# Kernel optimization log

Hardware: AMD Instinct MI355X
Metric: run time of the kernel (lower is better)

The kernel has to match this reference:

```python
import jax, jax.numpy as jnp
import numpy as np

B, S, H = 4, 2048, 2048
N_HEADS, KV_HEADS, RANK = 16, 8, 64
HEAD_DIM = H // N_HEADS          # 128
N_REP = N_HEADS // KV_HEADS      # 2
NEG = -1e9


def setup_inputs() -> dict:
    key = jax.random.key(0)
    ks = jax.random.split(key, 6)
    hidden_states = jax.random.normal(ks[0], (B, S, H), dtype=jnp.float32)
    # additive causal mask, broadcast over heads: [B,1,S,S]
    causal = jnp.tril(jnp.ones((S, S), dtype=bool))
    attention_mask = jnp.where(causal, 0.0, NEG).astype(jnp.float32)
    attention_mask = jnp.broadcast_to(attention_mask[None, None], (B, 1, S, S))
    sc = 1.0 / np.sqrt(H)
    Wq = jax.random.normal(ks[1], (H, RANK), dtype=jnp.float32) * sc
    Wk = jax.random.normal(ks[2], (H, RANK), dtype=jnp.float32) * sc
    Wv = jax.random.normal(ks[3], (H, KV_HEADS * HEAD_DIM), dtype=jnp.float32) * sc
    Wo = jax.random.normal(ks[4], (H, H), dtype=jnp.float32) * sc
    return {"hidden_states": hidden_states, "attention_mask": attention_mask,
            "Wq": Wq, "Wk": Wk, "Wv": Wv, "Wo": Wo}


def reference(hidden_states, attention_mask, Wq, Wk, Wv, Wo):
    b, s, h = hidden_states.shape
    # low-rank CP factors shared across heads: [B,S,R]
    q = hidden_states @ Wq
    k = hidden_states @ Wk
    # values with GQA: [B, kv_heads, S, head_dim] -> repeat to [B, n_heads, S, head_dim]
    v = (hidden_states @ Wv).reshape(b, s, KV_HEADS, HEAD_DIM).transpose(0, 2, 1, 3)
    v = jnp.repeat(v, N_REP, axis=1)
    # CP circuit over the (i,j) grid: scores[b,i,j] = sum_r q[b,i,r] * k[b,j,r]
    # (Hadamard over embedding factors gathered at grid indices, SumLayer with unit
    #  weights over rank; the all-ones head factor multiplies by 1). Head-shared.
    scores = jnp.einsum('bir,bjr->bij', q, k)[:, None]  # [B,1,S,S]
    scores = scores + attention_mask                     # additive causal mask
    probs = jax.nn.softmax(scores.astype(jnp.float32), axis=-1).astype(v.dtype)
    # attn_probs @ V, broadcasting the head-shared probs over heads
    ctx = jnp.einsum('bij,bhjd->bhid', probs[:, 0], v)   # [B,H,S,D]
    ctx = ctx.transpose(0, 2, 1, 3).reshape(b, s, h)
    return ctx @ Wo
```

## Files before the change

### kernel.cpp

```cpp
#include <hip/hip_runtime.h>

#define B_ 4
#define S_ 2048
#define H_ 2048
#define R_ 64
#define DKV_ 1024

typedef __attribute__((ext_vector_type(8))) short s16x8;
typedef __attribute__((ext_vector_type(4))) float f32x4v;

__device__ __forceinline__ unsigned short f2bf(float x) {
  unsigned int u = __builtin_bit_cast(unsigned int, x);
  u += 0x7FFF + ((u >> 16) & 1);
  return (unsigned short)(u >> 16);
}
__device__ __forceinline__ float bf2f(unsigned short h) {
  unsigned int u = ((unsigned int)h) << 16;
  return __builtin_bit_cast(float, u);
}

__device__ __forceinline__ void gl_lds16(const void* g, void* l) {
  __builtin_amdgcn_global_load_lds(
      (const __attribute__((address_space(1))) unsigned int*)g,
      (__attribute__((address_space(3))) unsigned int*)l, 16, 0, 0);
}

__device__ __forceinline__ int swz_off(int m, int kb) {
  int L = m >> 1;
  int slot = ((m & 1) << 2) | (kb >> 4);
  int sp = slot ^ (L & 7);
  return (L << 7) | (sp << 4) | (kb & 15);
}

__global__ __launch_bounds__(256) void k_f32_to_bf16x2(const float* __restrict__ in,
    unsigned short* __restrict__ hi, unsigned short* __restrict__ lo, int n4) {
  int i = blockIdx.x * 256 + threadIdx.x;
  if (i >= n4) return;
  float4 v = ((const float4*)in)[i];
  ushort4 h, l;
  h.x = f2bf(v.x); h.y = f2bf(v.y); h.z = f2bf(v.z); h.w = f2bf(v.w);
  l.x = f2bf(v.x - bf2f(h.x)); l.y = f2bf(v.y - bf2f(h.y));
  l.z = f2bf(v.z - bf2f(h.z)); l.w = f2bf(v.w - bf2f(h.w));
  ((ushort4*)hi)[i] = h;
  ((ushort4*)lo)[i] = l;
}

__global__ __launch_bounds__(256) void k_transpose_bf16(const float* __restrict__ in,
    unsigned short* __restrict__ out, int rows, int cols) {
  __shared__ float tile[32][33];
  int c0 = blockIdx.x * 32, r0 = blockIdx.y * 32;
  int tx = threadIdx.x & 31, ty = threadIdx.x >> 5;
  for (int i = 0; i < 4; ++i)
    tile[ty + i * 8][tx] = in[(size_t)(r0 + ty + i * 8) * cols + c0 + tx];
  __syncthreads();
  for (int i = 0; i < 4; ++i)
    out[(size_t)(c0 + ty + i * 8) * rows + r0 + tx] = f2bf(tile[tx][ty + i * 8]);
}

__global__ __launch_bounds__(256) void k_build_wqkt(const float* __restrict__ Wq,
    const float* __restrict__ Wk, unsigned short* __restrict__ hiT,
    unsigned short* __restrict__ loT) {
  __shared__ float tile[32][33];
  int k0 = blockIdx.x * 32, n0 = blockIdx.y * 32;
  const float* W = (n0 < 64) ? Wq : Wk;
  int nb = n0 & 63;
  int tx = threadIdx.x & 31, ty = threadIdx.x >> 5;
  for (int i = 0; i < 4; ++i)
    tile[ty + i * 8][tx] = W[(size_t)(k0 + ty + i * 8) * R_ + nb + tx];
  __syncthreads();
  for (int i = 0; i < 4; ++i) {
    float v = tile[tx][ty + i * 8];
    unsigned short h = f2bf(v);
    size_t idx = (size_t)(n0 + ty + i * 8) * H_ + k0 + tx;
    hiT[idx] = h;
    loT[idx] = f2bf(v - bf2f(h));
  }
}

__global__ __launch_bounds__(256) void k_build_wot(const float* __restrict__ Wo,
                                                   unsigned short* __restrict__ WoT) {
  __shared__ float tile[32][33];
  int n0 = blockIdx.x * 32, r0 = blockIdx.y * 32;
  int h1b = 256 * (r0 >> 7) + (r0 & 127);
  int tx = threadIdx.x & 31, ty = threadIdx.x >> 5;
  for (int i = 0; i < 4; ++i) {
    int dr = ty + i * 8;
    tile[dr][tx] = Wo[(size_t)(h1b + dr) * H_ + n0 + tx] +
                   Wo[(size_t)(h1b + 128 + dr) * H_ + n0 + tx];
  }
  __syncthreads();
  for (int i = 0; i < 4; ++i)
    WoT[(size_t)(n0 + ty + i * 8) * DKV_ + r0 + tx] = f2bf(tile[tx][ty + i * 8]);
}

__global__ __launch_bounds__(256) void k_qk_mfma(
    const unsigned short* __restrict__ Ahi, const unsigned short* __restrict__ Alo,
    const unsigned short* __restrict__ Bhi, const unsigned short* __restrict__ Blo,
    unsigned short* __restrict__ qkh, unsigned short* __restrict__ qkl) {
  constexpr int TQK = 20480;
  __shared__ __attribute__((aligned(16))) char lds[3 * TQK];
  int m0 = blockIdx.x * 32;
  int t = threadIdx.x;
  int lane = t & 63, wave = t >> 6;
  int lr = lane & 15, kb = (lane >> 4) << 4;

  auto stage = [&](int kt, int buf) {
    int k0 = kt << 5;
    char* base = &lds[buf * TQK];
    {
      int q = t & 127;
      int L = q >> 3;
      int slot = (q & 7) ^ (L & 7);
      int m = (L << 1) | (slot >> 2);
      int ke = (slot & 3) << 3;
      const unsigned short* src =
          (t < 128 ? Ahi : Alo) + (size_t)(m0 + m) * H_ + k0 + ke;
      gl_lds16(src, base + (t < 128 ? 0 : 2048) + q * 16);
    }
#pragma unroll
    for (int c = 0; c < 2; ++c) {
      int q = c * 256 + t;
      int L = q >> 3;
      int slot = (q & 7) ^ (L & 7);
      int n = (L << 1) | (slot >> 2);
      int ke = (slot & 3) << 3;
      gl_lds16(Bhi + (size_t)n * H_ + k0 + ke, base + 4096 + q * 16);
    }
#pragma unroll
    for (int c = 0; c < 2; ++c) {
      int q = c * 256 + t;
      int L = q >> 3;
      int slot = (q & 7) ^ (L & 7);
      int n = (L << 1) | (slot >> 2);
      int ke = (slot & 3) << 3;
      gl_lds16(Blo + (size_t)n * H_ + k0 + ke, base + 12288 + q * 16);
    }
  };

  f32x4v acc[2][2] = {};
  stage(0, 0);
  stage(1, 1);
  int cur = 0, nxt = 2;
  for (int kt = 0; kt < 64; ++kt) {
    __builtin_amdgcn_sched_barrier(0);
    if (kt < 63) asm volatile("s_waitcnt vmcnt(5)" ::: "memory");
    else asm volatile("s_waitcnt vmcnt(0)" ::: "memory");
    __builtin_amdgcn_s_barrier();
    __builtin_amdgcn_sched_barrier(0);
    if (kt + 2 < 64) stage(kt + 2, nxt);
    const char* base = &lds[cur * TQK];
    s16x8 ah[2], al[2], bh[2], bl[2];
#pragma unroll
    for (int m = 0; m < 2; ++m) {
      int o = swz_off(m * 16 + lr, kb);
      ah[m] = *(const s16x8*)(base + o);
      al[m] = *(const s16x8*)(base + 2048 + o);
    }
#pragma unroll
    for (int n = 0; n < 2; ++n) {
      int o = swz_off(wave * 32 + n * 16 + lr, kb);
      bh[n] = *(const s16x8*)(base + 4096 + o);
      bl[n] = *(const s16x8*)(base + 12288 + o);
    }
    __builtin_amdgcn_s_setprio(1);
#pragma unroll
    for (int m = 0; m < 2; ++m)
#pragma unroll
      for (int n = 0; n < 2; ++n) {
        acc[m][n] = __builtin_amdgcn_mfma_f32_16x16x32_bf16(ah[m], bh[n], acc[m][n], 0, 0, 0);
        acc[m][n] = __builtin_amdgcn_mfma_f32_16x16x32_bf16(ah[m], bl[n], acc[m][n], 0, 0, 0);
        acc[m][n] = __builtin_amdgcn_mfma_f32_16x16x32_bf16(al[m], bh[n], acc[m][n], 0, 0, 0);
      }
    __builtin_amdgcn_s_setprio(0);
    cur = (cur == 2) ? 0 : cur + 1;
    nxt = (nxt == 2) ? 0 : nxt + 1;
  }
  for (int m = 0; m < 2; ++m) {
    int lrow = m * 16 + ((lane >> 4) << 2);
    for (int n = 0; n < 2; ++n) {
      int lcol = wave * 32 + n * 16 + lr;
      for (int r = 0; r < 4; ++r) {
        float v = acc[m][n][r];
        unsigned short h = f2bf(v);
        size_t idx = (size_t)(m0 + lrow + r) * 128 + lcol;
        qkh[idx] = h;
        qkl[idx] = f2bf(v - bf2f(h));
      }
    }
  }
}

__global__ __launch_bounds__(512, 4) void k_attn_fused(
    const unsigned short* __restrict__ qkh, const unsigned short* __restrict__ qkl,
    const unsigned short* __restrict__ VT, unsigned short* __restrict__ ctx) {
  constexpr int TILEB = 24576;
  __shared__ __attribute__((aligned(16))) char lds[3 * TILEB + 4096 + 256];
  char* Pt = &lds[3 * TILEB];
  float* rs = (float*)&lds[3 * TILEB + 4096];

  int t = threadIdx.x;
  int gx = gridDim.x;
  int x = blockIdx.x;
  int bx = (x & 1) ? (gx - 1 - (x >> 1)) : (x >> 1);
  if (blockIdx.z & 2) bx = gx - 1 - bx;
  int z = blockIdx.z;
  int m0 = bx * 64, d0 = blockIdx.y * 256;

  int lane = t & 63, wave = t >> 6;
  int sm = wave >> 1, sn = wave & 1;
  int wr = wave >> 2, wc = wave & 3;
  int kb = (lane >> 4) << 4;

  const unsigned short* qh = qkh + (size_t)z * S_ * 128;
  const unsigned short* ql = qkl + (size_t)z * S_ * 128;

  s16x8 qfh[2], qfl[2];
  {
    size_t rq = (size_t)(m0 + sm * 16 + (lane & 15)) * 128 + ((lane >> 4) << 3);
    qfh[0] = *(const s16x8*)(qh + rq);
    qfh[1] = *(const s16x8*)(qh + rq + 32);
    qfl[0] = *(const s16x8*)(ql + rq);
    qfl[1] = *(const s16x8*)(ql + rq + 32);
  }

  auto stage = [&](int kt, int buf) {
    int j0 = kt << 5;
    char* base = &lds[buf * TILEB];
    {
      int q = t & 127;
      int L = q >> 3;
      int slot = (q & 7) ^ (L & 7);
      int jr = (L << 1) | (slot >> 2);
      int ke = (slot & 3) << 3;
      int sub = t >> 7;
      const unsigned short* src = ((sub < 2) ? qh : ql) +
          (size_t)(j0 + jr) * 128 + 64 + ((sub & 1) << 5) + ke;
      gl_lds16(src, base + sub * 2048 + q * 16);
    }
    char* vb = base + 8192;
#pragma unroll
    for (int c = 0; c < 2; ++c) {
      int q = c * 512 + t;
      int L = q >> 3;
      int slot = (q & 7) ^ (L & 7);
      int dr = (L << 1) | (slot >> 2);
      int ke = (slot & 3) << 3;
      gl_lds16(VT + (size_t)(d0 + dr) * (B_ * S_) + (size_t)z * S_ + j0 + ke,
               vb + q * 16);
    }
  };

  if (t < 64) rs[t] = 0.f;
  int NT = (m0 + 64) >> 5;
  stage(0, 0);
  stage(1, 1);

  int jrow = sn * 16 + (lane & 15);
  int koffs = swz_off(jrow, kb);
  int paoff[2], voff[4];
#pragma unroll
  for (int mf = 0; mf < 2; ++mf)
    paoff[mf] = swz_off(wr * 32 + mf * 16 + (lane & 15), kb);
#pragma unroll
  for (int nf = 0; nf < 4; ++nf)
    voff[nf] = swz_off(wc * 64 + nf * 16 + (lane & 15), kb);

  float ps[4] = {0.f, 0.f, 0.f, 0.f};
  f32x4v accp[2][4] = {};
  int prow = sm * 16 + ((lane >> 4) << 2);
  int pcol = sn * 16 + (lane & 15);

  int cur = 0, nxt = 2;
  for (int kt = 0; kt < NT; ++kt) {
    __builtin_amdgcn_sched_barrier(0);
    if (kt + 1 < NT) asm volatile("s_waitcnt vmcnt(3) lgkmcnt(0)" ::: "memory");
    else asm volatile("s_waitcnt vmcnt(0) lgkmcnt(0)" ::: "memory");
    __builtin_amdgcn_s_barrier();
    __builtin_amdgcn_sched_barrier(0);
    if (kt + 2 < NT) stage(kt + 2, nxt);
    const char* base = &lds[cur * TILEB];
    s16x8 kh[2], kl[2];
    kh[0] = *(const s16x8*)(base + koffs);
    kh[1] = *(const s16x8*)(base + 2048 + koffs);
    kl[0] = *(const s16x8*)(base + 4096 + koffs);
    kl[1] = *(const s16x8*)(base + 6144 + koffs);
    f32x4v s = {};
#pragma unroll
    for (int ks = 0; ks < 2; ++ks) {
      s = __builtin_amdgcn_mfma_f32_16x16x32_bf16(qfh[ks], kh[ks], s, 0, 0, 0);
      s = __builtin_amdgcn_mfma_f32_16x16x32_bf16(qfh[ks], kl[ks], s, 0, 0, 0);
      s = __builtin_amdgcn_mfma_f32_16x16x32_bf16(qfl[ks], kh[ks], s, 0, 0, 0);
    }
    int jg = (kt << 5) + pcol;
    int ig = m0 + prow;
#pragma unroll
    for (int r = 0; r < 4; ++r) {
      float p = (jg <= ig + r) ? __expf(s[r]) : 0.f;
      ps[r] += p;
      *(unsigned short*)(Pt + swz_off(prow + r, pcol * 2)) = f2bf(p);
    }
    __builtin_amdgcn_sched_barrier(0);
    asm volatile("s_waitcnt lgkmcnt(0)" ::: "memory");
    __builtin_amdgcn_s_barrier();
    __builtin_amdgcn_sched_barrier(0);
    s16x8 pa[2], vf[4];
#pragma unroll
    for (int mf = 0; mf < 2; ++mf) pa[mf] = *(const s16x8*)(Pt + paoff[mf]);
    const char* vbase = base + 8192;
#pragma unroll
    for (int nf = 0; nf < 4; ++nf) vf[nf] = *(const s16x8*)(vbase + voff[nf]);
    __builtin_amdgcn_s_setprio(1);
#pragma unroll
    for (int mf = 0; mf < 2; ++mf)
#pragma unroll
      for (int nf = 0; nf < 4; ++nf)
        accp[mf][nf] =
            __builtin_amdgcn_mfma_f32_16x16x32_bf16(pa[mf], vf[nf], accp[mf][nf], 0, 0, 0);
    __builtin_amdgcn_s_setprio(0);
    cur = (cur == 2) ? 0 : cur + 1;
    nxt = (nxt == 2) ? 0 : nxt + 1;
  }

#pragma unroll
  for (int r = 0; r < 4; ++r) {
    float v = ps[r];
    for (int msk = 1; msk < 16; msk <<= 1) v += __shfl_xor(v, msk, 64);
    if ((lane & 15) == 0) atomicAdd(&rs[prow + r], v);
  }
  __syncthreads();

  unsigned short* Cp = ctx + (size_t)(z * S_ + m0) * DKV_ + d0;
#pragma unroll
  for (int mf = 0; mf < 2; ++mf) {
    int lr0 = wr * 32 + mf * 16 + ((lane >> 4) << 2);
#pragma unroll
    for (int nf = 0; nf < 4; ++nf) {
      int lc = wc * 64 + nf * 16 + (lane & 15);
#pragma unroll
      for (int r = 0; r < 4; ++r) {
        float sc = 1.f / rs[lr0 + r];
        Cp[(size_t)(lr0 + r) * DKV_ + lc] = f2bf(accp[mf][nf][r] * sc);
      }
    }
  }
}

template <int BM, int BN, bool TRANS_OUT, bool OUT_BF16>
__global__ __launch_bounds__(512, 4) void k_gemm256(
    const unsigned short* __restrict__ A, int lda,
    const unsigned short* __restrict__ BT, int ldbt,
    void* __restrict__ C, int ldc, int K) {
  constexpr int ABYTES = BM * 64;
  constexpr int BBYTES = BN * 64;
  constexpr int TILEB = ABYTES + BBYTES;
  constexpr int WARPS_M = 4;
  constexpr int WARPS_N = 2;
  constexpr int WM = BM / WARPS_M;
  constexpr int WN = BN / WARPS_N;
  constexpr int MF = WM / 16;
  constexpr int NF = WN / 16;
  constexpr int LPS = BM / 128 + BN / 128;
  __shared__ __attribute__((aligned(16))) char lds[3 * TILEB];

  int t = threadIdx.x;
  int gx = gridDim.x;
  int id = blockIdx.y * gx + blockIdx.x;
  int cpx = gx >> 3;
  int xcd = id & 7, rr = id >> 3;
  int bx = xcd * cpx + rr % cpx;
  int by = rr / cpx;
  int m0 = bx * BM, n0 = by * BN;

  const unsigned short* Ab = A + (size_t)m0 * lda;
  const unsigned short* Bb = BT + (size_t)n0 * ldbt;

  int lane = t & 63, wave = t >> 6;
  int wr = wave / WARPS_N, wc = wave % WARPS_N;
  int kb = (lane >> 4) << 4;
  int aoff[MF], boff[NF];
#pragma unroll
  for (int mf = 0; mf < MF; ++mf)
    aoff[mf] = swz_off(wr * WM + mf * 16 + (lane & 15), kb);
#pragma unroll
  for (int nf = 0; nf < NF; ++nf)
    boff[nf] = swz_off(wc * WN + nf * 16 + (lane & 15), kb);

  int NT = K >> 5;

  auto stage = [&](int kt, int buf) {
    int k0 = kt << 5;
    char* la = &lds[buf * TILEB];
    char* lb = la + ABYTES;
#pragma unroll
    for (int c = 0; c < BM / 128; ++c) {
      int q = c * 512 + t;
      int L = q >> 3;
      int slot = (q & 7) ^ (L & 7);
      int m = (L << 1) | (slot >> 2);
      int ke = (slot & 3) << 3;
      gl_lds16(Ab + (size_t)m * lda + k0 + ke, la + q * 16);
    }
#pragma unroll
    for (int c = 0; c < BN / 128; ++c) {
      int q = c * 512 + t;
      int L = q >> 3;
      int slot = (q & 7) ^ (L & 7);
      int n = (L << 1) | (slot >> 2);
      int ke = (slot & 3) << 3;
      gl_lds16(Bb + (size_t)n * ldbt + k0 + ke, lb + q * 16);
    }
  };

  f32x4v acc[MF][NF] = {};
  stage(0, 0);
  if (NT > 1) stage(1, 1);
  int cur = 0, nxt = 2;
  for (int kt = 0; kt < NT; ++kt) {
    __builtin_amdgcn_sched_barrier(0);
    if (kt + 1 < NT) {
      if constexpr (LPS == 2) asm volatile("s_waitcnt vmcnt(2)" ::: "memory");
      else asm volatile("s_waitcnt vmcnt(3)" ::: "memory");
    } else {
      asm volatile("s_waitcnt vmcnt(0)" ::: "memory");
    }
    __builtin_amdgcn_s_barrier();
    __builtin_amdgcn_sched_barrier(0);
    if (kt + 2 < NT) stage(kt + 2, nxt);
    const char* la = &lds[cur * TILEB];
    const char* lb = la + ABYTES;
    s16x8 af[MF], bf[NF];
#pragma unroll
    for (int mf = 0; mf < MF; ++mf) af[mf] = *(const s16x8*)(la + aoff[mf]);
#pragma unroll
    for (int nf = 0; nf < NF; ++nf) bf[nf] = *(const s16x8*)(lb + boff[nf]);
    __builtin_amdgcn_s_setprio(1);
#pragma unroll
    for (int mf = 0; mf < MF; ++mf)
#pragma unroll
      for (int nf = 0; nf < NF; ++nf)
        acc[mf][nf] =
            __builtin_amdgcn_mfma_f32_16x16x32_bf16(af[mf], bf[nf], acc[mf][nf], 0, 0, 0);
    __builtin_amdgcn_s_setprio(0);
    cur = (cur == 2) ? 0 : cur + 1;
    nxt = (nxt == 2) ? 0 : nxt + 1;
  }

#pragma unroll
  for (int mf = 0; mf < MF; ++mf) {
    int lrow = wr * WM + mf * 16 + ((lane >> 4) << 2);
#pragma unroll
    for (int nf = 0; nf < NF; ++nf) {
      int lcol = wc * WN + nf * 16 + (lane & 15);
      f32x4v v = acc[mf][nf];
      if (TRANS_OUT) {
        ushort4 o;
        o.x = f2bf(v[0]); o.y = f2bf(v[1]); o.z = f2bf(v[2]); o.w = f2bf(v[3]);
        unsigned short* Cp = (unsigned short*)C;
        *(ushort4*)&Cp[(size_t)(n0 + lcol) * ldc + m0 + lrow] = o;
      } else {
#pragma unroll
        for (int r = 0; r < 4; ++r) {
          if (OUT_BF16) {
            unsigned short* Cp = (unsigned short*)C;
            Cp[(size_t)(m0 + lrow + r) * ldc + n0 + lcol] = f2bf(v[r]);
          } else {
            float* Cp = (float*)C;
            Cp[(size_t)(m0 + lrow + r) * ldc + n0 + lcol] = v[r];
          }
        }
      }
    }
  }
}

extern "C" void kernel_launch(void* const* d_in, const int* in_sizes, int n_in,
                              void* d_out, int out_size, void* d_ws, size_t ws_size,
                              hipStream_t stream) {
  const float* hs = (const float*)d_in[0];
  const float* Wq = (const float*)d_in[2];
  const float* Wk = (const float*)d_in[3];
  const float* Wv = (const float*)d_in[4];
  const float* Wo = (const float*)d_in[5];
  float* out = (float*)d_out;

  char* w = (char*)d_ws;
  unsigned short* hsb = (unsigned short*)w; w += (size_t)B_ * S_ * H_ * 2;
  unsigned short* hsl = (unsigned short*)w; w += (size_t)B_ * S_ * H_ * 2;
  unsigned short* WvT = (unsigned short*)w; w += (size_t)DKV_ * H_ * 2;
  unsigned short* WoT = (unsigned short*)w; w += (size_t)H_ * DKV_ * 2;
  unsigned short* WqkTh = (unsigned short*)w; w += (size_t)128 * H_ * 2;
  unsigned short* WqkTl = (unsigned short*)w; w += (size_t)128 * H_ * 2;
  unsigned short* VT  = (unsigned short*)w; w += (size_t)DKV_ * B_ * S_ * 2;
  unsigned short* ctx = (unsigned short*)w; w += (size_t)B_ * S_ * DKV_ * 2;
  unsigned short* qkh = (unsigned short*)w; w += (size_t)B_ * S_ * 128 * 2;
  unsigned short* qkl = (unsigned short*)w; w += (size_t)B_ * S_ * 128 * 2;

  k_f32_to_bf16x2<<<(B_ * S_ * H_ / 4 + 255) / 256, 256, 0, stream>>>(
      hs, hsb, hsl, B_ * S_ * H_ / 4);
  k_transpose_bf16<<<dim3(DKV_ / 32, H_ / 32), 256, 0, stream>>>(Wv, WvT, H_, DKV_);
  k_build_wot<<<dim3(H_ / 32, DKV_ / 32), 256, 0, stream>>>(Wo, WoT);
  k_build_wqkt<<<dim3(H_ / 32, 4), 256, 0, stream>>>(Wq, Wk, WqkTh, WqkTl);
  k_qk_mfma<<<B_ * S_ / 32, 256, 0, stream>>>(hsb, hsl, WqkTh, WqkTl, qkh, qkl);
  k_gemm256<256, 128, true, true>
      <<<dim3(B_ * S_ / 256, DKV_ / 128), 512, 0, stream>>>(
      hsb, H_, WvT, H_, VT, B_ * S_, H_);
  k_attn_fused<<<dim3(32, 4, B_), 512, 0, stream>>>(qkh, qkl, VT, ctx);
  k_gemm256<256, 128, false, false>
      <<<dim3(B_ * S_ / 256, H_ / 128), 512, 0, stream>>>(
      ctx, DKV_, WoT, DKV_, out, H_, DKV_);
}
```

Before: 201.8 us.

## Keep attention probabilities in registers via transposed QK MFMA feeding PV directly

The fused attention kernel now computes S^T (K as the A operand, Q as B), so each lane's score outputs already match the A-operand layout of a 16x16x16 bf16 MFMA. P can then feed the PV product straight from registers, with no LDS round-trip and no second block barrier per tile. Work is repartitioned so each wave owns 16 query rows and 128 output columns. Row sums are reduced with shuffles instead of LDS atomics, and the V tile now uses an unswizzled layout. The cost is redundant QK MFMAs (each wave recomputes the scores for its row block across the two column halves) and possible LDS bank conflicts on the narrower, unswizzled V reads.

Measured after the change: 225.6 us. +11.8%, slower.

```diff
diff --git a/kernel.cpp b/kernel.cpp
--- a/kernel.cpp
+++ b/kernel.cpp
@@ -7,6 +7,7 @@
 #define DKV_ 1024
 
 typedef __attribute__((ext_vector_type(8))) short s16x8;
+typedef __attribute__((ext_vector_type(4))) short s16x4;
 typedef __attribute__((ext_vector_type(4))) float f32x4v;
 
 __device__ __forceinline__ unsigned short f2bf(float x) {
@@ -194,9 +195,7 @@
     const unsigned short* __restrict__ qkh, const unsigned short* __restrict__ qkl,
     const unsigned short* __restrict__ VT, unsigned short* __restrict__ ctx) {
   constexpr int TILEB = 24576;
-  __shared__ __attribute__((aligned(16))) char lds[3 * TILEB + 4096 + 256];
-  char* Pt = &lds[3 * TILEB];
-  float* rs = (float*)&lds[3 * TILEB + 4096];
+  __shared__ __attribute__((aligned(16))) char lds[3 * TILEB];
 
   int t = threadIdx.x;
   int gx = gridDim.x;
@@ -207,8 +206,7 @@
   int m0 = bx * 64, d0 = blockIdx.y * 256;
 
   int lane = t & 63, wave = t >> 6;
-  int sm = wave >> 1, sn = wave & 1;
-  int wr = wave >> 2, wc = wave & 3;
+  int iq = wave & 3, wd = wave >> 2;
   int kb = (lane >> 4) << 4;
 
   const unsigned short* qh = qkh + (size_t)z * S_ * 128;
@@ -216,7 +214,7 @@
 
   s16x8 qfh[2], qfl[2];
   {
-    size_t rq = (size_t)(m0 + sm * 16 + (lane & 15)) * 128 + ((lane >> 4) << 3);
+    size_t rq = (size_t)(m0 + iq * 16 + (lane & 15)) * 128 + ((lane >> 4) << 3);
     qfh[0] = *(const s16x8*)(qh + rq);
     qfh[1] = *(const s16x8*)(qh + rq + 32);
     qfl[0] = *(const s16x8*)(ql + rq);
@@ -241,107 +239,89 @@
 #pragma unroll
     for (int c = 0; c < 2; ++c) {
       int q = c * 512 + t;
-      int L = q >> 3;
-      int slot = (q & 7) ^ (L & 7);
-      int dr = (L << 1) | (slot >> 2);
-      int ke = (slot & 3) << 3;
-      gl_lds16(VT + (size_t)(d0 + dr) * (B_ * S_) + (size_t)z * S_ + j0 + ke,
+      int dr = q >> 2, jc = (q & 3) << 3;
+      gl_lds16(VT + (size_t)(d0 + dr) * (B_ * S_) + (size_t)z * S_ + j0 + jc,
                vb + q * 16);
     }
   };
 
-  if (t < 64) rs[t] = 0.f;
   int NT = (m0 + 64) >> 5;
   stage(0, 0);
   stage(1, 1);
 
-  int jrow = sn * 16 + (lane & 15);
-  int koffs = swz_off(jrow, kb);
-  int paoff[2], voff[4];
-#pragma unroll
-  for (int mf = 0; mf < 2; ++mf)
-    paoff[mf] = swz_off(wr * 32 + mf * 16 + (lane & 15), kb);
-#pragma unroll
-  for (int nf = 0; nf < 4; ++nf)
-    voff[nf] = swz_off(wc * 64 + nf * 16 + (lane & 15), kb);
-
-  float ps[4] = {0.f, 0.f, 0.f, 0.f};
-  f32x4v accp[2][4] = {};
-  int prow = sm * 16 + ((lane >> 4) << 2);
-  int pcol = sn * 16 + (lane & 15);
+  int ko0 = swz_off(lane & 15, kb);
+  int ko1 = swz_off(16 + (lane & 15), kb);
+  float ps = 0.f;
+  f32x4v accp[8] = {};
+  int ig = m0 + iq * 16 + (lane & 15);
 
   int cur = 0, nxt = 2;
   for (int kt = 0; kt < NT; ++kt) {
     __builtin_amdgcn_sched_barrier(0);
-    if (kt + 1 < NT) asm volatile("s_waitcnt vmcnt(3) lgkmcnt(0)" ::: "memory");
-    else asm volatile("s_waitcnt vmcnt(0) lgkmcnt(0)" ::: "memory");
+    if (kt + 1 < NT) asm volatile("s_waitcnt vmcnt(3)" ::: "memory");
+    else asm volatile("s_waitcnt vmcnt(0)" ::: "memory");
     __builtin_amdgcn_s_barrier();
     __builtin_amdgcn_sched_barrier(0);
     if (kt + 2 < NT) stage(kt + 2, nxt);
     const char* base = &lds[cur * TILEB];
-    s16x8 kh[2], kl[2];
-    kh[0] = *(const s16x8*)(base + koffs);
-    kh[1] = *(const s16x8*)(base + 2048 + koffs);
-    kl[0] = *(const s16x8*)(base + 4096 + koffs);
-    kl[1] = *(const s16x8*)(base + 6144 + koffs);
-    f32x4v s = {};
-#pragma unroll
-    for (int ks = 0; ks < 2; ++ks) {
-      s = __builtin_amdgcn_mfma_f32_16x16x32_bf16(qfh[ks], kh[ks], s, 0, 0, 0);
-      s = __builtin_amdgcn_mfma_f32_16x16x32_bf16(qfh[ks], kl[ks], s, 0, 0, 0);
-      s = __builtin_amdgcn_mfma_f32_16x16x32_bf16(qfl[ks], kh[ks], s, 0, 0, 0);
-    }
-    int jg = (kt << 5) + pcol;
-    int ig = m0 + prow;
-#pragma unroll
-    for (int r = 0; r < 4; ++r) {
-      float p = (jg <= ig + r) ? __expf(s[r]) : 0.f;
-      ps[r] += p;
-      *(unsigned short*)(Pt + swz_off(prow + r, pcol * 2)) = f2bf(p);
-    }
-    __builtin_amdgcn_sched_barrier(0);
-    asm volatile("s_waitcnt lgkmcnt(0)" ::: "memory");
-    __builtin_amdgcn_s_barrier();
-    __builtin_amdgcn_sched_barrier(0);
-    s16x8 pa[2], vf[4];
-#pragma unroll
-    for (int mf = 0; mf < 2; ++mf) pa[mf] = *(const s16x8*)(Pt + paoff[mf]);
-    const char* vbase = base + 8192;
-#pragma unroll
-    for (int nf = 0; nf < 4; ++nf) vf[nf] = *(const s16x8*)(vbase + voff[nf]);
+    s16x4 pa[2];
+#pragma unroll
+    for (int h = 0; h < 2; ++h) {
+      int ko = h ? ko1 : ko0;
+      s16x8 kh0 = *(const s16x8*)(base + ko);
+      s16x8 kh1 = *(const s16x8*)(base + 2048 + ko);
+      s16x8 kl0 = *(const s16x8*)(base + 4096 + ko);
+      s16x8 kl1 = *(const s16x8*)(base + 6144 + ko);
+      f32x4v s = {};
+      s = __builtin_amdgcn_mfma_f32_16x16x32_bf16(kh0, qfh[0], s, 0, 0, 0);
+      s = __builtin_amdgcn_mfma_f32_16x16x32_bf16(kh1, qfh[1], s, 0, 0, 0);
+      s = __builtin_amdgcn_mfma_f32_16x16x32_bf16(kl0, qfh[0], s, 0, 0, 0);
+      s = __builtin_amdgcn_mfma_f32_16x16x32_bf16(kl1, qfh[1], s, 0, 0, 0);
+      s = __builtin_amdgcn_mfma_f32_16x16x32_bf16(kh0, qfl[0], s, 0, 0, 0);
+      s = __builtin_amdgcn_mfma_f32_16x16x32_bf16(kh1, qfl[1], s, 0, 0, 0);
+      int jb = (kt << 5) + h * 16 + ((lane >> 4) << 2);
+      s16x4 p;
+#pragma unroll
+      for (int r = 0; r < 4; ++r) {
+        float pv = (jb + r <= ig) ? __expf(s[r]) : 0.f;
+        ps += pv;
+        p[r] = (short)f2bf(pv);
+      }
+      pa[h] = p;
+    }
+    const char* vb = base + 8192;
+    int jby = (lane >> 4) << 3;
     __builtin_amdgcn_s_setprio(1);
 #pragma unroll
-    for (int mf = 0; mf < 2; ++mf)
-#pragma unroll
-      for (int nf = 0; nf < 4; ++nf)
-        accp[mf][nf] =
-            __builtin_amdgcn_mfma_f32_16x16x32_bf16(pa[mf], vf[nf], accp[mf][nf], 0, 0, 0);
+    for (int nf = 0; nf < 8; ++nf) {
+      int dl = wd * 128 + nf * 16 + (lane & 15);
+#pragma unroll
+      for (int h = 0; h < 2; ++h) {
+        s16x4 vf = *(const s16x4*)(vb + dl * 64 + h * 32 + jby);
+        asm volatile("v_mfma_f32_16x16x16_bf16 %0, %1, %2, %0"
+                     : "+v"(accp[nf]) : "v"(pa[h]), "v"(vf));
+      }
+    }
     __builtin_amdgcn_s_setprio(0);
     cur = (cur == 2) ? 0 : cur + 1;
     nxt = (nxt == 2) ? 0 : nxt + 1;
   }
 
-#pragma unroll
-  for (int r = 0; r < 4; ++r) {
-    float v = ps[r];
-    for (int msk = 1; msk < 16; msk <<= 1) v += __shfl_xor(v, msk, 64);
-    if ((lane & 15) == 0) atomicAdd(&rs[prow + r], v);
-  }
-  __syncthreads();
-
-  unsigned short* Cp = ctx + (size_t)(z * S_ + m0) * DKV_ + d0;
-#pragma unroll
-  for (int mf = 0; mf < 2; ++mf) {
-    int lr0 = wr * 32 + mf * 16 + ((lane >> 4) << 2);
-#pragma unroll
-    for (int nf = 0; nf < 4; ++nf) {
-      int lc = wc * 64 + nf * 16 + (lane & 15);
-#pragma unroll
-      for (int r = 0; r < 4; ++r) {
-        float sc = 1.f / rs[lr0 + r];
-        Cp[(size_t)(lr0 + r) * DKV_ + lc] = f2bf(accp[mf][nf][r] * sc);
-      }
-    }
+  ps += __shfl_xor(ps, 16, 64);
+  ps += __shfl_xor(ps, 32, 64);
+  float rcp[4];
+#pragma unroll
+  for (int r = 0; r < 4; ++r)
+    rcp[r] = 1.f / __shfl(ps, ((lane >> 4) << 2) + r, 64);
+
+  unsigned short* Cp = ctx + (size_t)(z * S_ + m0 + iq * 16) * DKV_ + d0 + wd * 128;
+  int r0 = (lane >> 4) << 2;
+#pragma unroll
+  for (int nf = 0; nf < 8; ++nf) {
+    int lc = nf * 16 + (lane & 15);
+#pragma unroll
+    for (int r = 0; r < 4; ++r)
+      Cp[(size_t)(r0 + r) * DKV_ + lc] = f2bf(accp[nf][r] * rcp[r]);
   }
 }
 
```

## Fuse fp32-to-bf16 hi/lo split of hidden states into the QK projection kernel

Applied to the files above, without the earlier changes.

Removes the standalone conversion kernel that wrote bf16 hi and lo copies of the hidden states. The QK projection kernel now loads fp32 hidden states through registers, splits them into hi/lo bf16, writes both into swizzled LDS, and stores the hi part to global for the later V GEMM. This drops one launch, the lo buffer and a full write+read pass over the activations. In exchange the A operand becomes a register-staged pipeline with conversion ALU work inside the MFMA loop and different waitcnt bookkeeping.

Result: no change. 199.5 us (-1.1%).

```diff
diff --git a/kernel.cpp b/kernel.cpp
--- a/kernel.cpp
+++ b/kernel.cpp
@@ -30,19 +30,6 @@
   int slot = ((m & 1) << 2) | (kb >> 4);
   int sp = slot ^ (L & 7);
   return (L << 7) | (sp << 4) | (kb & 15);
-}
-
-__global__ __launch_bounds__(256) void k_f32_to_bf16x2(const float* __restrict__ in,
-    unsigned short* __restrict__ hi, unsigned short* __restrict__ lo, int n4) {
-  int i = blockIdx.x * 256 + threadIdx.x;
-  if (i >= n4) return;
-  float4 v = ((const float4*)in)[i];
-  ushort4 h, l;
-  h.x = f2bf(v.x); h.y = f2bf(v.y); h.z = f2bf(v.z); h.w = f2bf(v.w);
-  l.x = f2bf(v.x - bf2f(h.x)); l.y = f2bf(v.y - bf2f(h.y));
-  l.z = f2bf(v.z - bf2f(h.z)); l.w = f2bf(v.w - bf2f(h.w));
-  ((ushort4*)hi)[i] = h;
-  ((ushort4*)lo)[i] = l;
 }
 
 __global__ __launch_bounds__(256) void k_transpose_bf16(const float* __restrict__ in,
@@ -93,9 +80,10 @@
     WoT[(size_t)(n0 + ty + i * 8) * DKV_ + r0 + tx] = f2bf(tile[tx][ty + i * 8]);
 }
 
-__global__ __launch_bounds__(256) void k_qk_mfma(
-    const unsigned short* __restrict__ Ahi, const unsigned short* __restrict__ Alo,
+__global__ __launch_bounds__(256) void k_qk_fused(
+    const float* __restrict__ hs,
     const unsigned short* __restrict__ Bhi, const unsigned short* __restrict__ Blo,
+    unsigned short* __restrict__ hsb,
     unsigned short* __restrict__ qkh, unsigned short* __restrict__ qkl) {
   constexpr int TQK = 20480;
   __shared__ __attribute__((aligned(16))) char lds[3 * TQK];
@@ -104,19 +92,14 @@
   int lane = t & 63, wave = t >> 6;
   int lr = lane & 15, kb = (lane >> 4) << 4;
 
-  auto stage = [&](int kt, int buf) {
+  int arow = t >> 3;
+  int acol = (t & 7) << 2;
+  const float* asrc = hs + (size_t)(m0 + arow) * H_ + acol;
+  unsigned short* hdst = hsb + (size_t)(m0 + arow) * H_ + acol;
+  int adst = swz_off(arow, ((t & 7) >> 1) << 4) + ((t & 1) << 3);
+
+  auto stageB = [&](int kt, char* base) {
     int k0 = kt << 5;
-    char* base = &lds[buf * TQK];
-    {
-      int q = t & 127;
-      int L = q >> 3;
-      int slot = (q & 7) ^ (L & 7);
-      int m = (L << 1) | (slot >> 2);
-      int ke = (slot & 3) << 3;
-      const unsigned short* src =
-          (t < 128 ? Ahi : Alo) + (size_t)(m0 + m) * H_ + k0 + ke;
-      gl_lds16(src, base + (t < 128 ? 0 : 2048) + q * 16);
-    }
 #pragma unroll
     for (int c = 0; c < 2; ++c) {
       int q = c * 256 + t;
@@ -137,17 +120,36 @@
     }
   };
 
+  auto convA = [&](const float4& v, char* wbuf, int kt) {
+    ushort4 h, l;
+    h.x = f2bf(v.x); h.y = f2bf(v.y); h.z = f2bf(v.z); h.w = f2bf(v.w);
+    l.x = f2bf(v.x - bf2f(h.x)); l.y = f2bf(v.y - bf2f(h.y));
+    l.z = f2bf(v.z - bf2f(h.z)); l.w = f2bf(v.w - bf2f(h.w));
+    *(ushort4*)(wbuf + adst) = h;
+    *(ushort4*)(wbuf + 2048 + adst) = l;
+    *(ushort4*)(hdst + (size_t)kt * 32) = h;
+  };
+
+  float4 Rcur, Rnext;
+  Rcur = *(const float4*)(asrc);
+  stageB(0, &lds[0]);
+  Rnext = *(const float4*)(asrc + 32);
+  stageB(1, &lds[TQK]);
+  convA(Rcur, &lds[0], 0);
+  Rcur = Rnext;
+
   f32x4v acc[2][2] = {};
-  stage(0, 0);
-  stage(1, 1);
-  int cur = 0, nxt = 2;
+  int cur = 0, wb = 1, sb = 2;
   for (int kt = 0; kt < 64; ++kt) {
     __builtin_amdgcn_sched_barrier(0);
-    if (kt < 63) asm volatile("s_waitcnt vmcnt(5)" ::: "memory");
-    else asm volatile("s_waitcnt vmcnt(0)" ::: "memory");
+    if (kt < 62) asm volatile("s_waitcnt vmcnt(6) lgkmcnt(0)" ::: "memory");
+    else asm volatile("s_waitcnt vmcnt(0) lgkmcnt(0)" ::: "memory");
     __builtin_amdgcn_s_barrier();
     __builtin_amdgcn_sched_barrier(0);
-    if (kt + 2 < 64) stage(kt + 2, nxt);
+    if (kt + 2 < 64) {
+      Rnext = *(const float4*)(asrc + (size_t)(kt + 2) * 32);
+      stageB(kt + 2, &lds[sb * TQK]);
+    }
     const char* base = &lds[cur * TQK];
     s16x8 ah[2], al[2], bh[2], bl[2];
 #pragma unroll
@@ -162,6 +164,7 @@
       bh[n] = *(const s16x8*)(base + 4096 + o);
       bl[n] = *(const s16x8*)(base + 12288 + o);
     }
+    if (kt + 1 < 64) convA(Rcur, &lds[wb * TQK], kt + 1);
     __builtin_amdgcn_s_setprio(1);
 #pragma unroll
     for (int m = 0; m < 2; ++m)
@@ -172,8 +175,10 @@
         acc[m][n] = __builtin_amdgcn_mfma_f32_16x16x32_bf16(al[m], bh[n], acc[m][n], 0, 0, 0);
       }
     __builtin_amdgcn_s_setprio(0);
+    Rcur = Rnext;
     cur = (cur == 2) ? 0 : cur + 1;
-    nxt = (nxt == 2) ? 0 : nxt + 1;
+    wb = (wb == 2) ? 0 : wb + 1;
+    sb = (sb == 2) ? 0 : sb + 1;
   }
   for (int m = 0; m < 2; ++m) {
     int lrow = m * 16 + ((lane >> 4) << 2);
@@ -485,7 +490,6 @@
 
   char* w = (char*)d_ws;
   unsigned short* hsb = (unsigned short*)w; w += (size_t)B_ * S_ * H_ * 2;
-  unsigned short* hsl = (unsigned short*)w; w += (size_t)B_ * S_ * H_ * 2;
   unsigned short* WvT = (unsigned short*)w; w += (size_t)DKV_ * H_ * 2;
   unsigned short* WoT = (unsigned short*)w; w += (size_t)H_ * DKV_ * 2;
   unsigned short* WqkTh = (unsigned short*)w; w += (size_t)128 * H_ * 2;
@@ -495,12 +499,10 @@
   unsigned short* qkh = (unsigned short*)w; w += (size_t)B_ * S_ * 128 * 2;
   unsigned short* qkl = (unsigned short*)w; w += (size_t)B_ * S_ * 128 * 2;
 
-  k_f32_to_bf16x2<<<(B_ * S_ * H_ / 4 + 255) / 256, 256, 0, stream>>>(
-      hs, hsb, hsl, B_ * S_ * H_ / 4);
   k_transpose_bf16<<<dim3(DKV_ / 32, H_ / 32), 256, 0, stream>>>(Wv, WvT, H_, DKV_);
   k_build_wot<<<dim3(H_ / 32, DKV_ / 32), 256, 0, stream>>>(Wo, WoT);
   k_build_wqkt<<<dim3(H_ / 32, 4), 256, 0, stream>>>(Wq, Wk, WqkTh, WqkTl);
-  k_qk_mfma<<<B_ * S_ / 32, 256, 0, stream>>>(hsb, hsl, WqkTh, WqkTl, qkh, qkl);
+  k_qk_fused<<<B_ * S_ / 32, 256, 0, stream>>>(hs, WqkTh, WqkTl, hsb, qkh, qkl);
   k_gemm256<256, 128, true, true>
       <<<dim3(B_ * S_ / 256, DKV_ / 128), 512, 0, stream>>>(
       hsb, H_, WvT, H_, VT, B_ * S_, H_);
```
